# Kernel optimization log

Hardware: AMD Instinct MI355X
Metric: run time of the kernel (lower is better)

Reference implementation:

```python
import jax, jax.numpy as jnp
import numpy as np

T, E, F, H, B = 3, 500000, 128, 64, 1024

def setup_inputs() -> dict:
    key = jax.random.key(0)
    k1, k2, k3, k4 = jax.random.split(key, 4)
    edge_attr = jax.random.normal(k1, (T, E, F), dtype=jnp.float32)
    batch = jax.random.randint(k2, (T, E), 0, B, dtype=jnp.int32)
    W1 = jax.random.normal(k3, (T, F, H), dtype=jnp.float32) * 0.08
    b1 = jnp.zeros((T, H), dtype=jnp.float32)
    W2 = jax.random.normal(k4, (T, H), dtype=jnp.float32) * 0.1
    b2 = jnp.zeros((T,), dtype=jnp.float32)
    return {"edge_attr": edge_attr, "batch": batch, "W1": W1, "b1": b1,
            "W2": W2, "b2": b2, "num_graphs": B}

def reference(edge_attr, batch, W1, b1, W2, b2, num_graphs):
    # Per edge type: MLP score -> per-graph segment softmax -> weighted scatter-sum.
    # Dropout is identity at eval time.
    def pool_one(ea, be, w1, bb1, w2, bb2):
        h = jnp.tanh(ea @ w1 + bb1)                 # [E, H]
        score = h @ w2 + bb2                        # [E]
        smax = jax.ops.segment_max(score, be, num_segments=num_graphs)  # [B]
        ex = jnp.exp(score - smax[be])              # stable softmax numerator
        ssum = jax.ops.segment_sum(ex, be, num_segments=num_graphs)    # [B]
        attn = ex / ssum[be]                        # [E]
        msgs = attn[:, None] * ea                   # [E, F]
        return jax.ops.segment_sum(msgs, be, num_segments=num_graphs)  # [B, F]
    pooled = jax.vmap(pool_one)(edge_attr, batch, W1, b1, W2, b2)      # [T, B, F]
    return pooled.mean(axis=0)                      # [B, F]
```

## Files before the change

kernel.cpp:

```cpp
#include <hip/hip_runtime.h>

#define T 3
#define E 500000
#define F 128
#define H 64
#define B 1024

#define BLK_E 64
#define EMASK 0x7FFFF
#define PB 1024

typedef __attribute__((ext_vector_type(4))) float f32x4;
typedef __fp16 h2 __attribute__((ext_vector_type(2)));
typedef __fp16 h8 __attribute__((ext_vector_type(8)));
union H4 {
  h2 p[2];
  uint2 d;
};
union HS {
  __fp16 h;
  unsigned short s;
};


__device__ __forceinline__ float tanh_fast(float x) {
  float e = __expf(2.0f * x);
  return 1.0f - 2.0f / (e + 1.0f);
}
__device__ __forceinline__ void bar_lds() {
  asm volatile("s_waitcnt lgkmcnt(0)" ::: "memory");
  __builtin_amdgcn_s_barrier();
  __builtin_amdgcn_sched_barrier(0);
}


__global__ void k_init(const float* __restrict__ W1, float* __restrict__ acc,
                       float* __restrict__ ssum, unsigned* __restrict__ cnt,
                       unsigned short* __restrict__ Wpack) {
  int idx = blockIdx.x * blockDim.x + threadIdx.x;
  if (idx < T * B * F) acc[idx] = 0.0f;
  if (idx < T * B) {
    ssum[idx] = 0.0f;
    cnt[idx] = 0u;
  }
  if (idx < T * 4 * 4 * 64) {
    int lane = idx & 63;
    int r2 = idx >> 6;
    int ks = r2 & 3;
    int nt = (r2 >> 2) & 3;
    int t = r2 >> 4;
    int j = nt * 16 + (lane & 15);
#pragma unroll
    for (int e = 0; e < 8; ++e) {
      int f = ks * 32 + (lane >> 4) * 8 + e;
      HS hs;
      hs.h = (__fp16)W1[((size_t)t * F + f) * H + j];
      Wpack[(size_t)idx * 8 + e] = hs.s;
    }
  }
}


__global__ __launch_bounds__(256) void k_hist(
    const int* __restrict__ batch, unsigned* __restrict__ cnt) {
  __shared__ unsigned h[B];
  int t = blockIdx.y;
  for (int i = threadIdx.x; i < B; i += 256) h[i] = 0u;
  __syncthreads();
  int base = blockIdx.x * 4096;
  int end = base + 4096 < E ? base + 4096 : E;
  for (int i = base + threadIdx.x; i < end; i += 256)
    atomicAdd(&h[batch[(size_t)t * E + i]], 1u);
  __syncthreads();
  for (int i = threadIdx.x; i < B; i += 256) {
    unsigned v = h[i];
    if (v) atomicAdd(&cnt[t * B + i], v);
  }
}


__global__ void k_scan(const unsigned* __restrict__ cnt,
                       unsigned* __restrict__ cursor) {
  __shared__ unsigned s[B];
  int tid = threadIdx.x;
  int t = blockIdx.x;
  unsigned v = cnt[t * B + tid];
  s[tid] = v;
  __syncthreads();
  for (int d = 1; d < B; d <<= 1) {
    unsigned x = (tid >= d) ? s[tid - d] : 0u;
    __syncthreads();
    s[tid] += x;
    __syncthreads();
  }
  cursor[t * B + tid] = s[tid] - v;
}


__global__ __launch_bounds__(256) void k_scatter(
    const int* __restrict__ batch, unsigned* __restrict__ cursor,
    unsigned* __restrict__ eid) {
  __shared__ unsigned hloc[B];
  __shared__ unsigned baseg[B];
  int t = blockIdx.y;
  int e = blockIdx.x * 256 + threadIdx.x;
  for (int i = threadIdx.x; i < B; i += 256) hloc[i] = 0u;
  __syncthreads();
  int b = 0;
  unsigned rank = 0;
  if (e < E) {
    b = batch[(size_t)t * E + e];
    rank = atomicAdd(&hloc[b], 1u);
  }
  __syncthreads();
  for (int i = threadIdx.x; i < B; i += 256) {
    unsigned cv = hloc[i];
    if (cv) baseg[i] = atomicAdd(&cursor[t * B + i], cv);
  }
  __syncthreads();
  if (e < E)
    eid[(size_t)t * E + baseg[b] + rank] = (unsigned)e | ((unsigned)b << 19);
}


__global__ __launch_bounds__(256, 3) void k_fused(
    const float* __restrict__ ea, const unsigned* __restrict__ eid,
    const unsigned short* __restrict__ Wpack, const float* __restrict__ b1,
    const float* __restrict__ W2, const float* __restrict__ b2,
    float* __restrict__ accg, float* __restrict__ ssum) {
  __shared__ unsigned short xh_t[BLK_E * F];
  __shared__ unsigned short xl_t[BLK_E * F];
  __shared__ float scl[BLK_E];
  __shared__ int eidl[3][BLK_E];
  __shared__ int bblb[3][BLK_E];

  int t = blockIdx.y;
  int tid = threadIdx.x;
  const int NT = (E + BLK_E - 1) / BLK_E;
  const int CH = (NT + PB - 1) / PB;
  int t0 = blockIdx.x * CH;
  int n = NT - t0;
  if (n <= 0) return;
  if (n > CH) n = CH;

  const float* eag = ea + (size_t)t * E * (size_t)F;
  const unsigned* eidt = eid + (size_t)t * E;
  int l = tid & 63;
  int w = tid >> 6;
  int c = tid & 31;
  int r0 = tid >> 5;
  int jb = l & 15;

  const unsigned short* wpt = Wpack + (size_t)t * 8192;
  h8 bh[4][4];
#pragma unroll
  for (int nt = 0; nt < 4; ++nt)
#pragma unroll
    for (int ks = 0; ks < 4; ++ks)
      bh[nt][ks] = *(const h8*)(wpt + ((nt * 4 + ks) * 64 + l) * 8);
  float b1r[4], w2r[4];
#pragma unroll
  for (int nt = 0; nt < 4; ++nt) {
    b1r[nt] = b1[t * H + nt * 16 + jb];
    w2r[nt] = W2[t * H + nt * 16 + jb];
  }
  float b2t = b2[t];

  if (tid < BLK_E) {
    int p0 = t0 * BLK_E + tid;
    if (p0 >= E) p0 = E - 1;
    unsigned pk = eidt[p0];
    eidl[0][tid] = (int)(pk & EMASK);
    bblb[0][tid] = (int)(pk >> 19);
    int p1 = (t0 + 1) * BLK_E + tid;
    if (p1 >= E) p1 = E - 1;
    pk = eidt[p1];
    eidl[1][tid] = (int)(pk & EMASK);
    bblb[1][tid] = (int)(pk >> 19);
  }
  __syncthreads();

  float4 v[8];
#pragma unroll
  for (int k = 0; k < 8; ++k) {
    int id = eidl[0][k * 8 + r0];
    v[k] = *(const float4*)(eag + (size_t)id * F + 4 * c);
  }

  int wv = tid >> 6;
  int ll = tid & 63;
  float* acct = accg + (size_t)t * B * F;
  float a0 = 0.f, a1 = 0.f, asum = 0.f;
  int prev = -1;

  for (int i = 0; i < n; ++i) {
    int ib = i % 3;
    int e0 = (t0 + i) * BLK_E;

#pragma unroll
    for (int k = 0; k < 8; ++k) {
      int r = k * 8 + r0;
      float4 x = v[k];
      H4 hv, lv;
      hv.p[0] = __builtin_amdgcn_cvt_pkrtz(x.x, x.y);
      hv.p[1] = __builtin_amdgcn_cvt_pkrtz(x.z, x.w);
      lv.p[0] = __builtin_amdgcn_cvt_pkrtz(x.x - (float)hv.p[0][0],
                                           x.y - (float)hv.p[0][1]);
      lv.p[1] = __builtin_amdgcn_cvt_pkrtz(x.z - (float)hv.p[1][0],
                                           x.w - (float)hv.p[1][1]);
      int off = (r * 256 + c * 8) ^ ((r & 7) << 4);
      *(uint2*)((char*)xh_t + off) = hv.d;
      *(uint2*)((char*)xl_t + off) = lv.d;
    }
    bar_lds();

    unsigned pk_next = 0;
    if (tid < BLK_E) {
      int p = (t0 + i + 2) * BLK_E + tid;
      if (p >= E) p = E - 1;
      pk_next = eidt[p];
    }
    if (i + 1 < n) {
      int nb = (i + 1) % 3;
#pragma unroll
      for (int k = 0; k < 8; ++k) {
        int id = eidl[nb][k * 8 + r0];
        v[k] = *(const float4*)(eag + (size_t)id * F + 4 * c);
      }
    }

    f32x4 acc[4];
#pragma unroll
    for (int nt = 0; nt < 4; ++nt) acc[nt] = (f32x4){0.f, 0.f, 0.f, 0.f};
    int arow = w * 16 + (l & 15);
    int abase = arow * 256;
    int aswz = (arow & 7) << 4;
#pragma unroll
    for (int ks = 0; ks < 4; ++ks) {
      int abyte = (abase + (ks * 32 + (l >> 4) * 8) * 2) ^ aswz;
      h8 ah = *(const h8*)((const char*)xh_t + abyte);
      h8 al = *(const h8*)((const char*)xl_t + abyte);
#pragma unroll
      for (int nt = 0; nt < 4; ++nt) {
        acc[nt] = __builtin_amdgcn_mfma_f32_16x16x32_f16(ah, bh[nt][ks],
                                                         acc[nt], 0, 0, 0);
        acc[nt] = __builtin_amdgcn_mfma_f32_16x16x32_f16(al, bh[nt][ks],
                                                         acc[nt], 0, 0, 0);
      }
    }

    float p0 = 0.f, p1 = 0.f, p2 = 0.f, p3 = 0.f;
#pragma unroll
    for (int nt = 0; nt < 4; ++nt) {
      p0 = fmaf(tanh_fast(acc[nt][0] + b1r[nt]), w2r[nt], p0);
      p1 = fmaf(tanh_fast(acc[nt][1] + b1r[nt]), w2r[nt], p1);
      p2 = fmaf(tanh_fast(acc[nt][2] + b1r[nt]), w2r[nt], p2);
      p3 = fmaf(tanh_fast(acc[nt][3] + b1r[nt]), w2r[nt], p3);
    }
#pragma unroll
    for (int m = 1; m < 16; m <<= 1) {
      p0 += __shfl_xor(p0, m);
      p1 += __shfl_xor(p1, m);
      p2 += __shfl_xor(p2, m);
      p3 += __shfl_xor(p3, m);
    }
    if (jb == 0) {
      int rb = w * 16 + (l >> 4) * 4;
      *(float4*)&scl[rb] = (float4){p0, p1, p2, p3};
    }
    bar_lds();

    for (int ii = 0; ii < 16; ++ii) {
      int eloc = wv * 16 + ii;
      if (e0 + eloc >= E) break;
      int b = bblb[ib][eloc];
      if (b != prev) {
        if (prev >= 0) {
          atomicAdd(acct + (size_t)prev * F + 2 * ll, a0);
          atomicAdd(acct + (size_t)prev * F + 2 * ll + 1, a1);
          if (ll == 0) atomicAdd(&ssum[t * B + prev], asum);
        }
        prev = b;
        a0 = 0.f;
        a1 = 0.f;
        asum = 0.f;
      }
      float exv = __expf(scl[eloc] + b2t);
      int off = (eloc * 256 + ll * 4) ^ ((eloc & 7) << 4);
      h2 xh = *(const h2*)((const char*)xh_t + off);
      h2 xl = *(const h2*)((const char*)xl_t + off);
      float x0 = (float)xh[0] + (float)xl[0];
      float x1 = (float)xh[1] + (float)xl[1];
      a0 = fmaf(x0, exv, a0);
      a1 = fmaf(x1, exv, a1);
      asum += exv;
    }

    if (tid < BLK_E) {
      eidl[(i + 2) % 3][tid] = (int)(pk_next & EMASK);
      bblb[(i + 2) % 3][tid] = (int)(pk_next >> 19);
    }
    bar_lds();
  }

  if (prev >= 0) {
    atomicAdd(acct + (size_t)prev * F + 2 * ll, a0);
    atomicAdd(acct + (size_t)prev * F + 2 * ll + 1, a1);
    if (ll == 0) atomicAdd(&ssum[t * B + prev], asum);
  }
}


__global__ __launch_bounds__(256) void k_final(
    const float* __restrict__ acc, const float* __restrict__ ssum,
    float* __restrict__ out) {
  int idx = blockIdx.x * 256 + threadIdx.x;
  if (idx >= B * F) return;
  int b = idx >> 7;
  float s = 0.0f;
#pragma unroll
  for (int t = 0; t < T; ++t)
    s += acc[(size_t)t * B * F + idx] / ssum[t * B + b];
  out[idx] = s * (1.0f / 3.0f);
}


extern "C" void kernel_launch(void* const* d_in, const int* in_sizes, int n_in,
                              void* d_out, int out_size, void* d_ws, size_t ws_size,
                              hipStream_t stream) {
  const float* ea    = (const float*)d_in[0];
  const int*   batch = (const int*)d_in[1];
  const float* W1    = (const float*)d_in[2];
  const float* b1    = (const float*)d_in[3];
  const float* W2    = (const float*)d_in[4];
  const float* b2    = (const float*)d_in[5];
  float* out = (float*)d_out;

  float*          acc    = (float*)d_ws;
  float*          ssum   = acc + (size_t)T * B * F;
  unsigned*       cnt    = (unsigned*)(ssum + T * B);
  unsigned*       cursor = cnt + T * B;
  unsigned*       eid    = cursor + T * B;
  unsigned short* Wpack  = (unsigned short*)(eid + (size_t)T * E);

  k_init<<<(T * B * F + 255) / 256, 256, 0, stream>>>(W1, acc, ssum, cnt, Wpack);

  dim3 gh((E + 4095) / 4096, T);
  k_hist<<<gh, 256, 0, stream>>>(batch, cnt);
  k_scan<<<T, B, 0, stream>>>(cnt, cursor);
  dim3 ge((E + 255) / 256, T);
  k_scatter<<<ge, 256, 0, stream>>>(batch, cursor, eid);

  dim3 gs(PB, T);
  k_fused<<<gs, 256, 0, stream>>>(ea, eid, Wpack, b1, W2, b2, acc, ssum);

  k_final<<<(B * F + 255) / 256, 256, 0, stream>>>(acc, ssum, out);
}
```

Baseline: 350.3 us.

## Split wavefront into two edge halves in scatter loop and memset workspace

The scatter-accumulate loop now has each wavefront handle two edges at once, with each half-wave covering all 128 features using 4 features per lane. This halves the serial loop trip count and widens the LDS reads to 8 bytes. Separately, zeroing of acc, ssum and cnt moves from the init kernel to hipMemsetAsync, leaving a small kernel that only packs W1. The price is more segment flushes, since each half tracks its own running segment and may issue extra atomics at graph boundaries.

```diff
diff --git a/kernel.cpp b/kernel.cpp
--- a/kernel.cpp
+++ b/kernel.cpp
@@ -34,15 +34,9 @@
 }
 
 
-__global__ void k_init(const float* __restrict__ W1, float* __restrict__ acc,
-                       float* __restrict__ ssum, unsigned* __restrict__ cnt,
+__global__ void k_pack(const float* __restrict__ W1,
                        unsigned short* __restrict__ Wpack) {
   int idx = blockIdx.x * blockDim.x + threadIdx.x;
-  if (idx < T * B * F) acc[idx] = 0.0f;
-  if (idx < T * B) {
-    ssum[idx] = 0.0f;
-    cnt[idx] = 0u;
-  }
   if (idx < T * 4 * 4 * 64) {
     int lane = idx & 63;
     int r2 = idx >> 6;
@@ -189,8 +183,11 @@
 
   int wv = tid >> 6;
   int ll = tid & 63;
+  int half = ll >> 5;
+  int q = ll & 31;
   float* acct = accg + (size_t)t * B * F;
-  float a0 = 0.f, a1 = 0.f, asum = 0.f;
+  float a4[4] = {0.f, 0.f, 0.f, 0.f};
+  float asum = 0.f;
   int prev = -1;
 
   for (int i = 0; i < n; ++i) {
@@ -270,30 +267,42 @@
     }
     bar_lds();
 
-    for (int ii = 0; ii < 16; ++ii) {
-      int eloc = wv * 16 + ii;
-      if (e0 + eloc >= E) break;
-      int b = bblb[ib][eloc];
-      if (b != prev) {
-        if (prev >= 0) {
-          atomicAdd(acct + (size_t)prev * F + 2 * ll, a0);
-          atomicAdd(acct + (size_t)prev * F + 2 * ll + 1, a1);
-          if (ll == 0) atomicAdd(&ssum[t * B + prev], asum);
+    for (int ii = 0; ii < 8; ++ii) {
+      int ebase = wv * 16 + 2 * ii;
+      if (e0 + ebase >= E) break;
+      int eloc = ebase + half;
+      if (e0 + eloc < E) {
+        int b = bblb[ib][eloc];
+        if (b != prev) {
+          if (prev >= 0) {
+            atomicAdd(acct + (size_t)prev * F + 4 * q + 0, a4[0]);
+            atomicAdd(acct + (size_t)prev * F + 4 * q + 1, a4[1]);
+            atomicAdd(acct + (size_t)prev * F + 4 * q + 2, a4[2]);
+            atomicAdd(acct + (size_t)prev * F + 4 * q + 3, a4[3]);
+            if (q == 0) atomicAdd(&ssum[t * B + prev], asum);
+          }
+          prev = b;
+          a4[0] = 0.f;
+          a4[1] = 0.f;
+          a4[2] = 0.f;
+          a4[3] = 0.f;
+          asum = 0.f;
         }
-        prev = b;
-        a0 = 0.f;
-        a1 = 0.f;
-        asum = 0.f;
+        float exv = __expf(scl[eloc] + b2t);
+        int off = (eloc * 256 + q * 8) ^ ((eloc & 7) << 4);
+        H4 xh, xl;
+        xh.d = *(const uint2*)((const char*)xh_t + off);
+        xl.d = *(const uint2*)((const char*)xl_t + off);
+        float x0 = (float)xh.p[0][0] + (float)xl.p[0][0];
+        float x1 = (float)xh.p[0][1] + (float)xl.p[0][1];
+        float x2 = (float)xh.p[1][0] + (float)xl.p[1][0];
+        float x3 = (float)xh.p[1][1] + (float)xl.p[1][1];
+        a4[0] = fmaf(x0, exv, a4[0]);
+        a4[1] = fmaf(x1, exv, a4[1]);
+        a4[2] = fmaf(x2, exv, a4[2]);
+        a4[3] = fmaf(x3, exv, a4[3]);
+        asum += exv;
       }
-      float exv = __expf(scl[eloc] + b2t);
-      int off = (eloc * 256 + ll * 4) ^ ((eloc & 7) << 4);
-      h2 xh = *(const h2*)((const char*)xh_t + off);
-      h2 xl = *(const h2*)((const char*)xl_t + off);
-      float x0 = (float)xh[0] + (float)xl[0];
-      float x1 = (float)xh[1] + (float)xl[1];
-      a0 = fmaf(x0, exv, a0);
-      a1 = fmaf(x1, exv, a1);
-      asum += exv;
     }
 
     if (tid < BLK_E) {
@@ -304,9 +313,11 @@
   }
 
   if (prev >= 0) {
-    atomicAdd(acct + (size_t)prev * F + 2 * ll, a0);
-    atomicAdd(acct + (size_t)prev * F + 2 * ll + 1, a1);
-    if (ll == 0) atomicAdd(&ssum[t * B + prev], asum);
+    atomicAdd(acct + (size_t)prev * F + 4 * q + 0, a4[0]);
+    atomicAdd(acct + (size_t)prev * F + 4 * q + 1, a4[1]);
+    atomicAdd(acct + (size_t)prev * F + 4 * q + 2, a4[2]);
+    atomicAdd(acct + (size_t)prev * F + 4 * q + 3, a4[3]);
+    if (q == 0) atomicAdd(&ssum[t * B + prev], asum);
   }
 }
 
@@ -343,7 +354,10 @@
   unsigned*       eid    = cursor + T * B;
   unsigned short* Wpack  = (unsigned short*)(eid + (size_t)T * E);
 
-  k_init<<<(T * B * F + 255) / 256, 256, 0, stream>>>(W1, acc, ssum, cnt, Wpack);
+  size_t zbytes = (size_t)T * B * F * 4 + (size_t)T * B * 4 * 3;
+  hipMemsetAsync(d_ws, 0, zbytes, stream);
+
+  k_pack<<<(T * 4 * 4 * 64 + 255) / 256, 256, 0, stream>>>(W1, Wpack);
 
   dim3 gh((E + 4095) / 4096, T);
   k_hist<<<gh, 256, 0, stream>>>(batch, cnt);
```

Result: slower. 368.2 us (+5.1%).
